# Kernel optimization log

Measured on AMD Instinct MI355X. Metric: run time of the kernel, lower is better.

Reference implementation:

```python
import jax, jax.numpy as jnp
import numpy as np

NUM_HEADS = 16


def setup_inputs() -> dict:
    rng = jax.random.key(0)
    ks = jax.random.split(rng, 11)
    T, B, E = 1024, 4, 1024
    s = E ** -0.5  # weight init scale
    return {
        "query": jax.random.normal(ks[0], (T, B, E), jnp.float32),
        "key": jax.random.normal(ks[1], (T, B, E), jnp.float32),
        "value": jax.random.normal(ks[2], (T, B, E), jnp.float32),
        "q_proj_weight": jax.random.normal(ks[3], (E, E), jnp.float32) * s,
        "k_proj_weight1": jax.random.normal(ks[4], (E, E), jnp.float32) * s,
        "k_proj_weight2": jax.random.normal(ks[5], (E, E), jnp.float32) * s,
        "v_proj_weight": jax.random.normal(ks[6], (E, E), jnp.float32) * s,
        "in_proj_bias": jax.random.normal(ks[7], (4 * E,), jnp.float32) * 0.02,
        "out_proj_weight": jax.random.normal(ks[8], (E, E), jnp.float32) * s,
        "out_proj_bias": jax.random.normal(ks[9], (E,), jnp.float32) * 0.02,
        "pi": jax.random.uniform(ks[10], (2, NUM_HEADS), jnp.float32, 0.3, 0.7),
    }


def reference(query, key, value, q_proj_weight, k_proj_weight1, k_proj_weight2,
              v_proj_weight, in_proj_bias, out_proj_weight, out_proj_bias, pi):
    T, Bz, E = query.shape
    H = NUM_HEADS
    hd = E // H
    scaling = hd ** -0.5

    b_q, b_k1, b_k2, b_v = jnp.split(in_proj_bias, 4)
    q = query @ q_proj_weight.T + b_q
    k1 = key @ k_proj_weight1.T + b_k1
    k2 = key @ k_proj_weight2.T + b_k2
    v = value @ v_proj_weight.T + b_v

    def heads(x):  # (S, B, E) -> (B*H, S, hd)
        S = x.shape[0]
        return x.reshape(S, Bz * H, hd).transpose(1, 0, 2)

    q, k1, k2, v = heads(q), heads(k1), heads(k2), heads(v)

    def sqdist(a, b):  # (B*H, Nt, hd), (B*H, Ns, hd) -> (B*H, Nt, Ns)
        a2 = jnp.sum(a * a, axis=-1)
        b2 = jnp.sum(b * b, axis=-1)
        ab = jnp.einsum('btd,bsd->bts', a, b)
        return a2[:, :, None] + b2[:, None, :] - 2.0 * ab

    e1 = jnp.exp(-scaling / 2.0 * sqdist(q, k1))
    e2 = jnp.exp(-3.0 * scaling / 2.0 * sqdist(q, k2))

    pi1 = jnp.clip(jnp.abs(pi[0]), 1e-6, 2.0)  # (H,)
    pi2 = jnp.clip(jnp.abs(pi[1]), 1e-6, 2.0)

    Nt, Ns = e1.shape[1], e1.shape[2]
    attn = (e1.reshape(Bz, H, Nt, Ns) * pi1[None, :, None, None]
            + e2.reshape(Bz, H, Nt, Ns) * pi2[None, :, None, None])
    attn = attn.reshape(Bz * H, Nt, Ns)
    attn = attn / (jnp.sum(attn, axis=-1, keepdims=True) + 1e-6)

    out = jnp.einsum('bts,bsd->btd', attn, v)        # (B*H, Nt, hd)
    out = out.transpose(1, 0, 2).reshape(T, Bz, E)   # (T, B, E)
    return out @ out_proj_weight.T + out_proj_bias
```

## Files before the change

### kernel.cpp

```cpp
#include <hip/hip_runtime.h>
#include <hip/hip_bf16.h>

#define T_DIM 1024
#define B_DIM 4
#define E_DIM 1024
#define H_DIM 16
#define HD    64
#define M_DIM (T_DIM * B_DIM)

typedef __hip_bfloat16 bf16;
typedef __bf16 bf16x8 __attribute__((ext_vector_type(8)));
typedef __bf16 bf16x4 __attribute__((ext_vector_type(4)));
typedef float  f32x4  __attribute__((ext_vector_type(4)));

#define P4S ((size_t)M_DIM * E_DIM)
#define P1S ((size_t)E_DIM * E_DIM)

__global__ __launch_bounds__(256) void cvt_all(
    const float* __restrict__ q, const float* __restrict__ k,
    const float* __restrict__ v, const float* __restrict__ w0,
    const float* __restrict__ w1, const float* __restrict__ w2,
    const float* __restrict__ w3, const float* __restrict__ w4,
    __bf16* __restrict__ dst)
{
  size_t i = ((size_t)blockIdx.x * 256 + threadIdx.x) * 8;
  const float* src;
  size_t off;
  if (i < P4S)            { src = q; off = i; }
  else if (i < 2 * P4S)   { src = k; off = i - P4S; }
  else if (i < 3 * P4S)   { src = v; off = i - 2 * P4S; }
  else {
    size_t j = i - 3 * P4S;
    int wsel = (int)(j >> 20);
    off = j & (P1S - 1);
    const float* ws[5] = {w0, w1, w2, w3, w4};
    src = ws[wsel];
  }
  float4 a = *(const float4*)(src + off);
  float4 b = *(const float4*)(src + off + 4);
  bf16x8 o;
  o[0] = (__bf16)a.x; o[1] = (__bf16)a.y; o[2] = (__bf16)a.z; o[3] = (__bf16)a.w;
  o[4] = (__bf16)b.x; o[5] = (__bf16)b.y; o[6] = (__bf16)b.z; o[7] = (__bf16)b.w;
  *(bf16x8*)(dst + i) = o;
}

__device__ __forceinline__ void load_lds16(const __bf16* g, __bf16* l) {
  __builtin_amdgcn_global_load_lds(
      (__attribute__((address_space(1))) void*)(void*)g,
      (__attribute__((address_space(3))) void*)l, 16, 0, 0);
}

__device__ __forceinline__ void stage_half(
    int H, const __bf16* __restrict__ X, const __bf16* __restrict__ W,
    int bm, int bn, __bf16* As, __bf16* Bs, int tid)
{
  if (H >= 64) return;
  const int T  = H >> 2;
  const int h  = H & 3;
  const int rh = (h & 1) * 128;
  const __bf16* src = (h < 2) ? X : W;
  const int rbase   = (h < 2) ? bm : bn;
  __bf16* lb = ((h < 2) ? As : Bs) + (T & 1) * 16384;
#pragma unroll
  for (int li = 0; li < 2; ++li) {
    int r  = rh + li * 64 + (tid >> 3);
    int gc = (tid & 7) ^ (r & 7);
    load_lds16(src + (size_t)(rbase + r) * E_DIM + T * 64 + gc * 8,
               lb + (rh + li * 64) * 64 + tid * 8);
  }
}

#define RD(base, row, c) \
  (*(const bf16x8*)((base) + (row) * 64 + ((((c) ^ ((row) & 7))) << 3)))

__global__ __launch_bounds__(512, 2) void proj_gemm4(
    const __bf16* __restrict__ xbase, const __bf16* __restrict__ wbase,
    const float* __restrict__ bin, __bf16* __restrict__ cbase)
{
  __shared__ __bf16 lds[65536];
  __bf16* As = lds;
  __bf16* Bs = lds + 32768;

  const int z = blockIdx.z;
  const __bf16* X = xbase + ((z == 0) ? 0 : (z == 3) ? 2 * P4S : P4S);
  const __bf16* W = wbase + (size_t)z * P1S;
  const float* bias = bin + z * E_DIM;
  __bf16* C = cbase + (size_t)z * P4S;

  const int bm = blockIdx.x * 256;
  const int bn = blockIdx.y * 256;

  const int tid  = threadIdx.x;
  const int lane = tid & 63;
  const int w    = tid >> 6;
  const int wm   = w >> 2;
  const int wn   = w & 3;
  const int mrow = lane & 15, quad = lane >> 4;

  f32x4 acc[8][4];
#pragma unroll
  for (int m = 0; m < 8; ++m)
#pragma unroll
    for (int n = 0; n < 4; ++n) acc[m][n] = (f32x4)0.0f;

#pragma unroll
  for (int H = 0; H < 5; ++H) stage_half(H, X, W, bm, bn, As, Bs, tid);
  asm volatile("s_waitcnt vmcnt(2)" ::: "memory");
  __builtin_amdgcn_s_barrier();

  bf16x8 af[4][2];
  bf16x8 bq[4][2];

#pragma unroll 2
  for (int t = 0; t < 16; ++t) {
    const __bf16* Ab = As + (t & 1) * 16384;
    const __bf16* Bb = Bs + (t & 1) * 16384;

#pragma unroll
    for (int n = 0; n < 2; ++n)
#pragma unroll
      for (int kk = 0; kk < 2; ++kk)
        bq[n][kk] = RD(Bb, wn * 64 + n * 16 + mrow, kk * 4 + quad);
#pragma unroll
    for (int m = 0; m < 4; ++m)
#pragma unroll
      for (int kk = 0; kk < 2; ++kk)
        af[m][kk] = RD(Ab, wm * 128 + m * 16 + mrow, kk * 4 + quad);
    stage_half(4 * t + 5, X, W, bm, bn, As, Bs, tid);
    __builtin_amdgcn_s_barrier();
    asm volatile("s_waitcnt lgkmcnt(0)" ::: "memory");
    __builtin_amdgcn_s_setprio(1);
#pragma unroll
    for (int kk = 0; kk < 2; ++kk)
#pragma unroll
      for (int n = 0; n < 2; ++n)
#pragma unroll
        for (int m = 0; m < 4; ++m)
          acc[m][n] = __builtin_amdgcn_mfma_f32_16x16x32_bf16(
              af[m][kk], bq[n][kk], acc[m][n], 0, 0, 0);
    __builtin_amdgcn_s_setprio(0);
    __builtin_amdgcn_s_barrier();

#pragma unroll
    for (int n = 2; n < 4; ++n)
#pragma unroll
      for (int kk = 0; kk < 2; ++kk)
        bq[n][kk] = RD(Bb, wn * 64 + n * 16 + mrow, kk * 4 + quad);
    stage_half(4 * t + 6, X, W, bm, bn, As, Bs, tid);
    __builtin_amdgcn_s_barrier();
    asm volatile("s_waitcnt lgkmcnt(0)" ::: "memory");
    __builtin_amdgcn_s_setprio(1);
#pragma unroll
    for (int kk = 0; kk < 2; ++kk)
#pragma unroll
      for (int n = 2; n < 4; ++n)
#pragma unroll
        for (int m = 0; m < 4; ++m)
          acc[m][n] = __builtin_amdgcn_mfma_f32_16x16x32_bf16(
              af[m][kk], bq[n][kk], acc[m][n], 0, 0, 0);
    __builtin_amdgcn_s_setprio(0);
    __builtin_amdgcn_s_barrier();

#pragma unroll
    for (int m = 0; m < 4; ++m)
#pragma unroll
      for (int kk = 0; kk < 2; ++kk)
        af[m][kk] = RD(Ab, wm * 128 + 64 + m * 16 + mrow, kk * 4 + quad);
    stage_half(4 * t + 7, X, W, bm, bn, As, Bs, tid);
    __builtin_amdgcn_s_barrier();
    asm volatile("s_waitcnt lgkmcnt(0)" ::: "memory");
    __builtin_amdgcn_s_setprio(1);
#pragma unroll
    for (int kk = 0; kk < 2; ++kk)
#pragma unroll
      for (int n = 0; n < 2; ++n)
#pragma unroll
        for (int m = 0; m < 4; ++m)
          acc[4 + m][n] = __builtin_amdgcn_mfma_f32_16x16x32_bf16(
              af[m][kk], bq[n][kk], acc[4 + m][n], 0, 0, 0);
    __builtin_amdgcn_s_setprio(0);
    __builtin_amdgcn_s_barrier();

    stage_half(4 * t + 8, X, W, bm, bn, As, Bs, tid);
    __builtin_amdgcn_s_barrier();
    __builtin_amdgcn_s_setprio(1);
#pragma unroll
    for (int kk = 0; kk < 2; ++kk)
#pragma unroll
      for (int n = 2; n < 4; ++n)
#pragma unroll
        for (int m = 0; m < 4; ++m)
          acc[4 + m][n] = __builtin_amdgcn_mfma_f32_16x16x32_bf16(
              af[m][kk], bq[n][kk], acc[4 + m][n], 0, 0, 0);
    __builtin_amdgcn_s_setprio(0);
    if (t < 14)       { asm volatile("s_waitcnt vmcnt(2)" ::: "memory"); }
    else if (t == 14) { asm volatile("s_waitcnt vmcnt(0)" ::: "memory"); }
    __builtin_amdgcn_s_barrier();
  }

#pragma unroll
  for (int n = 0; n < 4; ++n) {
    int col = bn + wn * 64 + n * 16 + mrow;
    float bc = bias[col];
#pragma unroll
    for (int m = 0; m < 8; ++m) {
      int rbase = bm + wm * 128 + m * 16 + quad * 4;
#pragma unroll
      for (int r = 0; r < 4; ++r)
        C[(size_t)(rbase + r) * E_DIM + col] = (__bf16)(acc[m][n][r] + bc);
    }
  }
}

template <typename TO>
__device__ __forceinline__ void gemm_body(
    const __bf16* __restrict__ X, const __bf16* __restrict__ W,
    const float* __restrict__ bias, TO* __restrict__ C,
    int bm, int bn, int Ndim, int Kdim, __bf16* As, __bf16* Bs)
{
  const int tid  = threadIdx.x;
  const int lane = tid & 63;
  const int wave = tid >> 6;
  const int wy = (wave >> 1) * 64;
  const int wx = (wave & 1) * 64;
  const int mrow = lane & 15, quad = lane >> 4;

  const int srow = tid >> 2;
  const int ke   = (tid & 3) * 8;
  const __bf16* gA0 = X + (size_t)(bm + srow)      * Kdim + ke;
  const __bf16* gA1 = X + (size_t)(bm + srow + 64) * Kdim + ke;
  const __bf16* gB0 = W + (size_t)(bn + srow)      * Kdim + ke;
  const __bf16* gB1 = W + (size_t)(bn + srow + 64) * Kdim + ke;
  __bf16* lA0 = As + tid * 8;
  __bf16* lA1 = As + (tid + 256) * 8;
  __bf16* lB0 = Bs + tid * 8;
  __bf16* lB1 = Bs + (tid + 256) * 8;

  f32x4 acc[4][4];
#pragma unroll
  for (int i = 0; i < 4; ++i)
#pragma unroll
    for (int j = 0; j < 4; ++j) acc[i][j] = (f32x4)0.0f;

  for (int k0 = 0; k0 < Kdim; k0 += 32) {
    __syncthreads();
    load_lds16(gA0 + k0, lA0);
    load_lds16(gA1 + k0, lA1);
    load_lds16(gB0 + k0, lB0);
    load_lds16(gB1 + k0, lB1);
    __syncthreads();
    bf16x8 af[4], bf[4];
#pragma unroll
    for (int i = 0; i < 4; ++i)
      af[i] = *(const bf16x8*)(As + (wy + i * 16 + mrow) * 32 + quad * 8);
#pragma unroll
    for (int j = 0; j < 4; ++j)
      bf[j] = *(const bf16x8*)(Bs + (wx + j * 16 + mrow) * 32 + quad * 8);
#pragma unroll
    for (int i = 0; i < 4; ++i)
#pragma unroll
      for (int j = 0; j < 4; ++j)
        acc[i][j] = __builtin_amdgcn_mfma_f32_16x16x32_bf16(af[i], bf[j], acc[i][j], 0, 0, 0);
  }

#pragma unroll
  for (int j = 0; j < 4; ++j) {
    int col = bn + wx + j * 16 + mrow;
    float bc = bias[col];
#pragma unroll
    for (int i = 0; i < 4; ++i) {
      int rbase = bm + wy + i * 16 + quad * 4;
#pragma unroll
      for (int r = 0; r < 4; ++r)
        C[(size_t)(rbase + r) * Ndim + col] = (TO)(acc[i][j][r] + bc);
    }
  }
}

__global__ __launch_bounds__(256) void out_gemm(
    const __bf16* __restrict__ X, const __bf16* __restrict__ W,
    const float* __restrict__ bias, float* __restrict__ C)
{
  __shared__ __bf16 As[128 * 32];
  __shared__ __bf16 Bs[128 * 32];
  gemm_body<float>(X, W, bias, C, blockIdx.x * 128, blockIdx.y * 128,
                   E_DIM, E_DIM, As, Bs);
}

__global__ __launch_bounds__(256) void norms_vt(
    const __bf16* __restrict__ Qp, const __bf16* __restrict__ K1p,
    const __bf16* __restrict__ K2p, const __bf16* __restrict__ Vp,
    float* __restrict__ qn, float* __restrict__ kn1, float* __restrict__ kn2,
    __bf16* __restrict__ Vt_g)
{
  __shared__ __bf16 tile[64][88];
  const int tid = threadIdx.x;
  if (blockIdx.x < 768) {
    int id = blockIdx.x * 256 + tid;
    int which = id >> 16;
    int r = id & 65535;
    int bh = r >> 10, t = r & 1023;
    int b = bh >> 4, h = bh & 15;
    const __bf16* src = (which == 0) ? Qp : ((which == 1) ? K1p : K2p);
    float* dst = (which == 0) ? qn : ((which == 1) ? kn1 : kn2);
    const __bf16* p = src + (size_t)(t * 4 + b) * 1024 + h * 64;
    float s = 0.f;
#pragma unroll
    for (int c = 0; c < 8; ++c) {
      bf16x8 v = *(const bf16x8*)(p + c * 8);
#pragma unroll
      for (int j = 0; j < 8; ++j) { float x = (float)v[j]; s += x * x; }
    }
    dst[bh * 1024 + t] = s;
    return;
  }
  int bid = blockIdx.x - 768;
  const int bh = bid & 63, kt = bid >> 6;
  const int b = bh >> 4, h = bh & 15;
  {
    int s = tid >> 2, d0 = (tid & 3) * 16;
    const __bf16* src = Vp + (size_t)((kt * 64 + s) * 4 + b) * 1024 + h * 64 + d0;
    *(bf16x8*)(&tile[s][d0])     = *(const bf16x8*)(src);
    *(bf16x8*)(&tile[s][d0 + 8]) = *(const bf16x8*)(src + 8);
  }
  __syncthreads();
#pragma unroll
  for (int c = 0; c < 2; ++c) {
    int idx = tid * 2 + c;
    int d = idx >> 3, u0 = (idx & 7) * 8;
    bf16x8 o;
#pragma unroll
    for (int i = 0; i < 8; ++i) {
      int u = u0 + i;
      int s = (u & 3) * 16 + (u >> 2);
      o[i] = tile[s][d];
    }
    *(bf16x8*)(Vt_g + ((size_t)bh * 64 + d) * 1024 + kt * 64 + u0) = o;
  }
}

__global__ __launch_bounds__(256, 4) void mgk_attn_mfma(
    const __bf16* __restrict__ Qp, const __bf16* __restrict__ K1p,
    const __bf16* __restrict__ K2p, const __bf16* __restrict__ Vt_g,
    const float* __restrict__ qn_g, const float* __restrict__ kn1_g,
    const float* __restrict__ kn2_g, const float* __restrict__ pi,
    __bf16* __restrict__ AO)
{
  __shared__ __bf16 lds[16384];
  __bf16* K1s = lds;
  __bf16* K2s = lds + 4096;
  __bf16* Vt  = lds + 8192;
  __bf16* Pl  = lds + 12288;

  const int bh = blockIdx.x, qt = blockIdx.y;
  const int b = bh >> 4, h = bh & 15;
  const int tid = threadIdx.x, lane = tid & 63, w = tid >> 6;
  const int mrow = lane & 15, quad = lane >> 4;

  const float cl1 = 0.0625f * 1.4426950408889634f;
  const float cl2 = 0.1875f * 1.4426950408889634f;
  const float L1 = 2.0f * cl1, L2 = 2.0f * cl2;
  const float p1 = fminf(fmaxf(fabsf(pi[h]), 1e-6f), 2.0f);
  const float p2 = fminf(fmaxf(fabsf(pi[H_DIM + h]), 1e-6f), 2.0f);
  const float lp1 = __log2f(p1), lp2 = __log2f(p2);
  const int hoff = h * 64;

  bf16x8 af[2];
  {
    const __bf16* qp = Qp + (size_t)((qt * 64 + w * 16 + mrow) * 4 + b) * 1024
                       + hoff + quad * 8;
    af[0] = *(const bf16x8*)(qp);
    af[1] = *(const bf16x8*)(qp + 32);
  }
  f32x4 qnv = *(const f32x4*)(qn_g + bh * 1024 + qt * 64 + w * 16 + quad * 4);
  f32x4 aq2;
#pragma unroll
  for (int r = 0; r < 4; ++r) aq2[r] = fmaf(cl1 - cl2, qnv[r], lp2);

  const int lw = lane >> 3;
  const int c  = lane & 7;
  const int dsw  = (c ^ lw) << 3;
  const int dstA = (w * 2) * 512 + lw * 64 + dsw;
  const int dstB = (w * 2 + 1) * 512 + lw * 64 + dsw;
  const int kr0 = w * 16 + lw, kr1 = kr0 + 8;

  const size_t KSTRIDE = (size_t)64 * 4 * 1024;
  const __bf16* pk1a = K1p + (size_t)(kr0 * 4 + b) * 1024 + hoff + c * 8;
  const __bf16* pk1b = K1p + (size_t)(kr1 * 4 + b) * 1024 + hoff + c * 8;
  const __bf16* pk2a = K2p + (size_t)(kr0 * 4 + b) * 1024 + hoff + c * 8;
  const __bf16* pk2b = K2p + (size_t)(kr1 * 4 + b) * 1024 + hoff + c * 8;
  const __bf16* pva  = Vt_g + ((size_t)bh * 64 + kr0) * 1024 + c * 8;
  const __bf16* pvb  = Vt_g + ((size_t)bh * 64 + kr1) * 1024 + c * 8;
  const float*  pn1  = kn1_g + bh * 1024 + mrow;
  const float*  pn2  = kn2_g + bh * 1024 + mrow;

  bf16x8 fk1a, fk1b, fk2a, fk2b, fva, fvb;
  float fn1[4], fn2[4];
  fk1a = *(const bf16x8*)pk1a; fk1b = *(const bf16x8*)pk1b;
  fk2a = *(const bf16x8*)pk2a; fk2b = *(const bf16x8*)pk2b;
  fva  = *(const bf16x8*)pva;  fvb  = *(const bf16x8*)pvb;
#pragma unroll
  for (int j = 0; j < 4; ++j) { fn1[j] = pn1[j * 16]; fn2[j] = pn2[j * 16]; }

  f32x4 oacc[4];
#pragma unroll
  for (int j = 0; j < 4; ++j) oacc[j] = (f32x4)0.0f;
  f32x4 rsl = (f32x4)0.0f;

  for (int kt = 0; kt < 16; ++kt) {
    __syncthreads();
    *(bf16x8*)(K1s + dstA) = fk1a;  *(bf16x8*)(K1s + dstB) = fk1b;
    *(bf16x8*)(K2s + dstA) = fk2a;  *(bf16x8*)(K2s + dstB) = fk2b;
    *(bf16x8*)(Vt  + dstA) = fva;   *(bf16x8*)(Vt  + dstB) = fvb;
    float nb1[4], s2[4];
#pragma unroll
    for (int j = 0; j < 4; ++j) {
      nb1[j] = fmaf(-cl1, fn1[j], lp1);
      s2[j]  = -cl2 * fn2[j];
    }
    if (kt < 15) {
      pk1a += KSTRIDE; pk1b += KSTRIDE; pk2a += KSTRIDE; pk2b += KSTRIDE;
      pva += 64; pvb += 64; pn1 += 64; pn2 += 64;
      fk1a = *(const bf16x8*)pk1a; fk1b = *(const bf16x8*)pk1b;
      fk2a = *(const bf16x8*)pk2a; fk2b = *(const bf16x8*)pk2b;
      fva  = *(const bf16x8*)pva;  fvb  = *(const bf16x8*)pvb;
#pragma unroll
      for (int j = 0; j < 4; ++j) { fn1[j] = pn1[j * 16]; fn2[j] = pn2[j * 16]; }
    }
    asm volatile("s_waitcnt lgkmcnt(0)" ::: "memory");
    __builtin_amdgcn_s_barrier();

    f32x4 acc1[4], acc2[4];
#pragma unroll
    for (int j = 0; j < 4; ++j) { acc1[j] = (f32x4)0.0f; acc2[j] = (f32x4)0.0f; }
#pragma unroll
    for (int kk = 0; kk < 2; ++kk)
#pragma unroll
      for (int j = 0; j < 4; ++j) {
        bf16x8 b1f = *(const bf16x8*)(K1s + (j * 16 + mrow) * 64
                                      + (((kk * 4 + quad) ^ (mrow & 7)) << 3));
        bf16x8 b2f = *(const bf16x8*)(K2s + (j * 16 + mrow) * 64
                                      + (((kk * 4 + quad) ^ (mrow & 7)) << 3));
        acc1[j] = __builtin_amdgcn_mfma_f32_16x16x32_bf16(af[kk], b1f, acc1[j], 0, 0, 0);
        acc2[j] = __builtin_amdgcn_mfma_f32_16x16x32_bf16(af[kk], b2f, acc2[j], 0, 0, 0);
      }

    f32x4 pv[4];
#pragma unroll
    for (int j = 0; j < 4; ++j) {
      f32x4 p;
#pragma unroll
      for (int r = 0; r < 4; ++r) {
        float e1 = __builtin_amdgcn_exp2f(fmaf(L1, acc1[j][r], nb1[j]));
        float e2 = __builtin_amdgcn_exp2f(fmaf(L2, acc2[j][r], s2[j] + aq2[r]));
        p[r] = e1 + e2;
      }
      pv[j] = p;
      rsl += p;
    }
#pragma unroll
    for (int r = 0; r < 4; ++r) {
      int q = quad * 4 + r;
      bf16x4 pk;
      pk[0] = (__bf16)pv[0][r]; pk[1] = (__bf16)pv[1][r];
      pk[2] = (__bf16)pv[2][r]; pk[3] = (__bf16)pv[3][r];
      int lc = mrow >> 1;
      *(bf16x4*)(Pl + w * 1024 + q * 64 + ((lc ^ (q & 7)) << 3) + (mrow & 1) * 4) = pk;
    }

    bf16x8 pf[2];
#pragma unroll
    for (int kk = 0; kk < 2; ++kk)
      pf[kk] = *(const bf16x8*)(Pl + w * 1024 + mrow * 64
                                + (((kk * 4 + quad) ^ (mrow & 7)) << 3));
#pragma unroll
    for (int kk = 0; kk < 2; ++kk)
#pragma unroll
      for (int j = 0; j < 4; ++j) {
        bf16x8 vf = *(const bf16x8*)(Vt + (j * 16 + mrow) * 64
                                     + (((kk * 4 + quad) ^ (mrow & 7)) << 3));
        oacc[j] = __builtin_amdgcn_mfma_f32_16x16x32_bf16(pf[kk], vf, oacc[j], 0, 0, 0);
      }
  }

#pragma unroll
  for (int d = 1; d < 16; d <<= 1) {
    f32x4 o;
#pragma unroll
    for (int r = 0; r < 4; ++r) o[r] = __shfl_xor(rsl[r], d, 64);
    rsl += o;
  }

  f32x4 inv;
#pragma unroll
  for (int r = 0; r < 4; ++r) inv[r] = 1.0f / (rsl[r] + 1e-6f);
#pragma unroll
  for (int j = 0; j < 4; ++j) {
    int col = hoff + j * 16 + mrow;
#pragma unroll
    for (int r = 0; r < 4; ++r) {
      int t = qt * 64 + w * 16 + quad * 4 + r;
      AO[(size_t)(t * 4 + b) * 1024 + col] = (__bf16)(oacc[j][r] * inv[r]);
    }
  }
}

extern "C" void kernel_launch(void* const* d_in, const int* in_sizes, int n_in,
                              void* d_out, int out_size, void* d_ws, size_t ws_size,
                              hipStream_t stream) {
  const float* query = (const float*)d_in[0];
  const float* key   = (const float*)d_in[1];
  const float* value = (const float*)d_in[2];
  const float* Wq    = (const float*)d_in[3];
  const float* Wk1   = (const float*)d_in[4];
  const float* Wk2   = (const float*)d_in[5];
  const float* Wv    = (const float*)d_in[6];
  const float* bin   = (const float*)d_in[7];
  const float* Wo    = (const float*)d_in[8];
  const float* bo    = (const float*)d_in[9];
  const float* pi    = (const float*)d_in[10];
  float* out = (float*)d_out;

  __bf16* qc  = (__bf16*)d_ws;
  __bf16* wq  = qc  + 3 * P4S;
  __bf16* wo  = wq  + 4 * P1S;
  __bf16* Qp  = wq  + 5 * P1S;
  __bf16* K1p = Qp  + P4S;
  __bf16* K2p = K1p + P4S;
  __bf16* Vp  = K2p + P4S;
  __bf16* AO  = Vp  + P4S;
  float*  qn_g  = (float*)(AO + P4S);
  float*  kn1_g = qn_g  + 64 * 1024;
  float*  kn2_g = kn1_g + 64 * 1024;
  __bf16* Vt_g  = qc;

  cvt_all<<<8704, 256, 0, stream>>>(query, key, value, Wq, Wk1, Wk2, Wv, Wo, qc);

  proj_gemm4<<<dim3(M_DIM / 256, E_DIM / 256, 4), 512, 0, stream>>>(qc, wq, bin, Qp);

  norms_vt<<<768 + 1024, 256, 0, stream>>>(Qp, K1p, K2p, Vp,
                                           qn_g, kn1_g, kn2_g, Vt_g);

  mgk_attn_mfma<<<dim3(64, 16), 256, 0, stream>>>(
      Qp, K1p, K2p, Vt_g, qn_g, kn1_g, kn2_g, pi, AO);

  out_gemm<<<dim3(M_DIM / 128, E_DIM / 128), 256, 0, stream>>>(AO, wo, bo, out);
}
```

Measured before the change: 257.9 us.

## Double-buffer K/V tiles with direct global-to-LDS loads and 128-row query blocks

The attention kernel now runs 512 threads per block covering 128 query rows, so each K1/K2/Vt tile is loaded once and shared by twice as many rows. The old register-staged prefetch (global to registers, then LDS stores behind a barrier) is replaced by direct global-to-LDS loads into two alternating buffers, issued two tiles ahead and gated by vmcnt waits. Key norms are now read from global memory inside the loop, and the MFMA sections are wrapped in s_setprio. The cost is 64 KB of LDS per block, which halves the number of blocks and limits how many fit on each CU.

```diff
diff --git a/kernel.cpp b/kernel.cpp
--- a/kernel.cpp
+++ b/kernel.cpp
@@ -339,18 +339,15 @@
   }
 }
 
-__global__ __launch_bounds__(256, 4) void mgk_attn_mfma(
+__global__ __launch_bounds__(512, 4) void mgk_attn_mfma(
     const __bf16* __restrict__ Qp, const __bf16* __restrict__ K1p,
     const __bf16* __restrict__ K2p, const __bf16* __restrict__ Vt_g,
     const float* __restrict__ qn_g, const float* __restrict__ kn1_g,
     const float* __restrict__ kn2_g, const float* __restrict__ pi,
     __bf16* __restrict__ AO)
 {
-  __shared__ __bf16 lds[16384];
-  __bf16* K1s = lds;
-  __bf16* K2s = lds + 4096;
-  __bf16* Vt  = lds + 8192;
-  __bf16* Pl  = lds + 12288;
+  __shared__ __bf16 lds[32768];
+  __bf16* Pl = lds + 24576;
 
   const int bh = blockIdx.x, qt = blockIdx.y;
   const int b = bh >> 4, h = bh & 15;
@@ -367,40 +364,36 @@
 
   bf16x8 af[2];
   {
-    const __bf16* qp = Qp + (size_t)((qt * 64 + w * 16 + mrow) * 4 + b) * 1024
+    const __bf16* qp = Qp + (size_t)((qt * 128 + w * 16 + mrow) * 4 + b) * 1024
                        + hoff + quad * 8;
     af[0] = *(const bf16x8*)(qp);
     af[1] = *(const bf16x8*)(qp + 32);
   }
-  f32x4 qnv = *(const f32x4*)(qn_g + bh * 1024 + qt * 64 + w * 16 + quad * 4);
+  f32x4 qnv = *(const f32x4*)(qn_g + bh * 1024 + qt * 128 + w * 16 + quad * 4);
   f32x4 aq2;
 #pragma unroll
   for (int r = 0; r < 4; ++r) aq2[r] = fmaf(cl1 - cl2, qnv[r], lp2);
 
-  const int lw = lane >> 3;
-  const int c  = lane & 7;
-  const int dsw  = (c ^ lw) << 3;
-  const int dstA = (w * 2) * 512 + lw * 64 + dsw;
-  const int dstB = (w * 2 + 1) * 512 + lw * 64 + dsw;
-  const int kr0 = w * 16 + lw, kr1 = kr0 + 8;
-
-  const size_t KSTRIDE = (size_t)64 * 4 * 1024;
-  const __bf16* pk1a = K1p + (size_t)(kr0 * 4 + b) * 1024 + hoff + c * 8;
-  const __bf16* pk1b = K1p + (size_t)(kr1 * 4 + b) * 1024 + hoff + c * 8;
-  const __bf16* pk2a = K2p + (size_t)(kr0 * 4 + b) * 1024 + hoff + c * 8;
-  const __bf16* pk2b = K2p + (size_t)(kr1 * 4 + b) * 1024 + hoff + c * 8;
-  const __bf16* pva  = Vt_g + ((size_t)bh * 64 + kr0) * 1024 + c * 8;
-  const __bf16* pvb  = Vt_g + ((size_t)bh * 64 + kr1) * 1024 + c * 8;
-  const float*  pn1  = kn1_g + bh * 1024 + mrow;
-  const float*  pn2  = kn2_g + bh * 1024 + mrow;
-
-  bf16x8 fk1a, fk1b, fk2a, fk2b, fva, fvb;
-  float fn1[4], fn2[4];
-  fk1a = *(const bf16x8*)pk1a; fk1b = *(const bf16x8*)pk1b;
-  fk2a = *(const bf16x8*)pk2a; fk2b = *(const bf16x8*)pk2b;
-  fva  = *(const bf16x8*)pva;  fvb  = *(const bf16x8*)pvb;
-#pragma unroll
-  for (int j = 0; j < 4; ++j) { fn1[j] = pn1[j * 16]; fn2[j] = pn2[j * 16]; }
+  const int srow = tid >> 3;
+  const int sc   = tid & 7;
+  const int gc   = sc ^ (srow & 7);
+  const int doff = tid * 8;
+  const __bf16* gK1 = K1p + (size_t)(srow * 4 + b) * 1024 + hoff + gc * 8;
+  const __bf16* gK2 = K2p + (size_t)(srow * 4 + b) * 1024 + hoff + gc * 8;
+  const __bf16* gVt = Vt_g + ((size_t)bh * 64 + srow) * 1024 + gc * 8;
+
+#define STAGE_T(kt_, bsel_) do {                                         \
+    __bf16* bb_ = lds + (bsel_) * 12288;                                 \
+    load_lds16(gK1 + (size_t)(kt_) * 262144, bb_ + doff);                \
+    load_lds16(gK2 + (size_t)(kt_) * 262144, bb_ + 4096 + doff);         \
+    load_lds16(gVt + (kt_) * 64,             bb_ + 8192 + doff);         \
+  } while (0)
+
+  STAGE_T(0, 0);
+  STAGE_T(1, 1);
+  asm volatile("s_waitcnt vmcnt(3)" ::: "memory");
+  __builtin_amdgcn_s_barrier();
+  asm volatile("" ::: "memory");
 
   f32x4 oacc[4];
 #pragma unroll
@@ -408,31 +401,24 @@
   f32x4 rsl = (f32x4)0.0f;
 
   for (int kt = 0; kt < 16; ++kt) {
-    __syncthreads();
-    *(bf16x8*)(K1s + dstA) = fk1a;  *(bf16x8*)(K1s + dstB) = fk1b;
-    *(bf16x8*)(K2s + dstA) = fk2a;  *(bf16x8*)(K2s + dstB) = fk2b;
-    *(bf16x8*)(Vt  + dstA) = fva;   *(bf16x8*)(Vt  + dstB) = fvb;
+    const int cur = kt & 1;
+    const __bf16* K1s = lds + cur * 12288;
+    const __bf16* K2s = K1s + 4096;
+    const __bf16* Vt  = K1s + 8192;
+
     float nb1[4], s2[4];
 #pragma unroll
     for (int j = 0; j < 4; ++j) {
-      nb1[j] = fmaf(-cl1, fn1[j], lp1);
-      s2[j]  = -cl2 * fn2[j];
-    }
-    if (kt < 15) {
-      pk1a += KSTRIDE; pk1b += KSTRIDE; pk2a += KSTRIDE; pk2b += KSTRIDE;
-      pva += 64; pvb += 64; pn1 += 64; pn2 += 64;
-      fk1a = *(const bf16x8*)pk1a; fk1b = *(const bf16x8*)pk1b;
-      fk2a = *(const bf16x8*)pk2a; fk2b = *(const bf16x8*)pk2b;
-      fva  = *(const bf16x8*)pva;  fvb  = *(const bf16x8*)pvb;
-#pragma unroll
-      for (int j = 0; j < 4; ++j) { fn1[j] = pn1[j * 16]; fn2[j] = pn2[j * 16]; }
-    }
-    asm volatile("s_waitcnt lgkmcnt(0)" ::: "memory");
-    __builtin_amdgcn_s_barrier();
+      float f1 = kn1_g[bh * 1024 + kt * 64 + j * 16 + mrow];
+      float f2 = kn2_g[bh * 1024 + kt * 64 + j * 16 + mrow];
+      nb1[j] = fmaf(-cl1, f1, lp1);
+      s2[j]  = -cl2 * f2;
+    }
 
     f32x4 acc1[4], acc2[4];
 #pragma unroll
     for (int j = 0; j < 4; ++j) { acc1[j] = (f32x4)0.0f; acc2[j] = (f32x4)0.0f; }
+    __builtin_amdgcn_s_setprio(1);
 #pragma unroll
     for (int kk = 0; kk < 2; ++kk)
 #pragma unroll
@@ -444,6 +430,7 @@
         acc1[j] = __builtin_amdgcn_mfma_f32_16x16x32_bf16(af[kk], b1f, acc1[j], 0, 0, 0);
         acc2[j] = __builtin_amdgcn_mfma_f32_16x16x32_bf16(af[kk], b2f, acc2[j], 0, 0, 0);
       }
+    __builtin_amdgcn_s_setprio(0);
 
     f32x4 pv[4];
 #pragma unroll
@@ -473,6 +460,7 @@
     for (int kk = 0; kk < 2; ++kk)
       pf[kk] = *(const bf16x8*)(Pl + w * 1024 + mrow * 64
                                 + (((kk * 4 + quad) ^ (mrow & 7)) << 3));
+    __builtin_amdgcn_s_setprio(1);
 #pragma unroll
     for (int kk = 0; kk < 2; ++kk)
 #pragma unroll
@@ -481,7 +469,22 @@
                                      + (((kk * 4 + quad) ^ (mrow & 7)) << 3));
         oacc[j] = __builtin_amdgcn_mfma_f32_16x16x32_bf16(pf[kk], vf, oacc[j], 0, 0, 0);
       }
-  }
+    __builtin_amdgcn_s_setprio(0);
+
+    if (kt < 15) {
+      asm volatile("s_waitcnt lgkmcnt(0)" ::: "memory");
+      __builtin_amdgcn_s_barrier();
+      if (kt < 14) {
+        STAGE_T(kt + 2, cur);
+        asm volatile("s_waitcnt vmcnt(3)" ::: "memory");
+      } else {
+        asm volatile("s_waitcnt vmcnt(0)" ::: "memory");
+      }
+      __builtin_amdgcn_s_barrier();
+      asm volatile("" ::: "memory");
+    }
+  }
+#undef STAGE_T
 
 #pragma unroll
   for (int d = 1; d < 16; d <<= 1) {
@@ -499,7 +502,7 @@
     int col = hoff + j * 16 + mrow;
 #pragma unroll
     for (int r = 0; r < 4; ++r) {
-      int t = qt * 64 + w * 16 + quad * 4 + r;
+      int t = qt * 128 + w * 16 + quad * 4 + r;
       AO[(size_t)(t * 4 + b) * 1024 + col] = (__bf16)(oacc[j][r] * inv[r]);
     }
   }
@@ -541,7 +544,7 @@
   norms_vt<<<768 + 1024, 256, 0, stream>>>(Qp, K1p, K2p, Vp,
                                            qn_g, kn1_g, kn2_g, Vt_g);
 
-  mgk_attn_mfma<<<dim3(64, 16), 256, 0, stream>>>(
+  mgk_attn_mfma<<<dim3(64, 8), 512, 0, stream>>>(
       Qp, K1p, K2p, Vt_g, qn_g, kn1_g, kn2_g, pi, AO);
 
   out_gemm<<<dim3(M_DIM / 128, E_DIM / 128), 256, 0, stream>>>(AO, wo, bo, out);
```

New measurement: 238.3 us. 1.08x faster.
